# Performance work log

Hardware: AMD Instinct MI355X
Metric: run time of the kernel (lower is better)

The kernel has to match this reference:

```python
import jax, jax.numpy as jnp
import numpy as np

N, M, E, DIM, H = 50000, 50000, 640000, 128, 8
DH = DIM // H
EPS = 1e-5

def _prelu(x, alpha):
    return jnp.where(x >= 0, x, alpha * x)

def setup_inputs() -> dict:
    key0 = jax.random.key(0)
    ks = jax.random.split(key0, 12)
    s = 1.0 / np.sqrt(DIM)
    return {
        "query": jax.random.normal(ks[0], (N, DIM), jnp.float32),
        "key": jax.random.normal(ks[1], (M, DIM), jnp.float32),
        "value": jax.random.normal(ks[2], (M, DIM), jnp.float32),
        "query_idx": jax.random.randint(ks[3], (E,), 0, N),
        "key_idx": jax.random.randint(ks[4], (E,), 0, M),
        "Wq": jax.random.normal(ks[5], (DIM, DIM), jnp.float32) * s,
        "bq": jnp.zeros((DIM,), jnp.float32),
        "Wk": jax.random.normal(ks[6], (DIM, DIM), jnp.float32) * s,
        "bk": jnp.zeros((DIM,), jnp.float32),
        "Wv": jax.random.normal(ks[7], (DIM, DIM), jnp.float32) * s,
        "bv": jnp.zeros((DIM,), jnp.float32),
        "Wp": jax.random.normal(ks[8], (DIM, DIM), jnp.float32) * s,
        "bp": jnp.zeros((DIM,), jnp.float32),
        "a": jax.random.normal(ks[9], (1, H, DH), jnp.float32) * 0.1,
        "alpha": jnp.full((1,), 0.25, jnp.float32),
        "gamma": jnp.ones((DIM,), jnp.float32),
        "beta": jnp.zeros((DIM,), jnp.float32),
    }

def reference(query, key, value, query_idx, key_idx, Wq, bq, Wk, bk, Wv, bv, Wp, bp, a, alpha, gamma, beta):
    n = query.shape[0]
    # projections (node-level, then gather per edge; linear commutes with gather)
    Qq = query @ Wq + bq            # [N, DIM]
    Kq = query @ Wk + bk            # [N, DIM] (self-attn key)
    Kk = key @ Wk + bk              # [M, DIM]
    Vq = query @ Wv + bv            # [N, DIM]
    Vv = value @ Wv + bv            # [M, DIM]
    # self-attention score per query node: [N, H, 1]
    attn_qq = (a * _prelu(Qq + Kq, alpha).reshape(n, H, DH)).sum(-1, keepdims=True)
    # per-edge additive attention score: [E, H, 1]
    e_feat = _prelu(Qq[query_idx] + Kk[key_idx], alpha)
    attn_e = (a * e_feat.reshape(-1, H, DH)).sum(-1, keepdims=True)
    # stable softmax over irregular query groups (include self)
    max_attn = jax.lax.stop_gradient(attn_qq.at[query_idx].max(attn_e))
    exp_qq = jnp.exp(attn_qq - max_attn)                 # [N, H, 1]
    exp_e = jnp.exp(attn_e - max_attn[query_idx])        # [E, H, 1]
    denom = exp_qq.at[query_idx].add(exp_e)              # [N, H, 1]
    denom = jnp.where(denom == 0, 1.0, denom)
    # weighted value scatter-sum (value_idx == key_idx)
    msg = exp_qq * Vq.reshape(n, H, DH)
    msg = msg.at[query_idx].add(exp_e * Vv[key_idx].reshape(-1, H, DH))
    out = (msg / denom).reshape(n, DIM) @ Wp + bp
    res = query + out
    mu = res.mean(-1, keepdims=True)
    var = res.var(-1, keepdims=True)
    return gamma * (res - mu) / jnp.sqrt(var + EPS) + beta
```

## Files before the change

kernel.cpp:

```cpp
#include <hip/hip_runtime.h>
#include <math.h>

#define DIM 128
#define NH 8
#define LN_EPS 1e-5f
#define NEGINF -3.0e38f

using bf16x8 = __attribute__((ext_vector_type(8))) short;
using f32x4  = __attribute__((ext_vector_type(4))) float;

__device__ __forceinline__ float prelu_f(float x, float al) { return x >= 0.f ? x : al * x; }

__device__ __forceinline__ short f2bf(float f) {
    unsigned u = __float_as_uint(f);
    unsigned r = (u + 0x7fffu + ((u >> 16) & 1u)) >> 16;
    return (short)r;
}
__device__ __forceinline__ float bflo(unsigned u) { return __uint_as_float(u << 16); }
__device__ __forceinline__ float bfhi(unsigned u) { return __uint_as_float(u & 0xffff0000u); }

__device__ __forceinline__ unsigned cvt_pk_bf16(float lo, float hi) {
    unsigned r;
    asm("v_cvt_pk_bf16_f32 %0, %1, %2" : "=v"(r) : "v"(lo), "v"(hi));
    return r;
}

__device__ __forceinline__ float swz_xor1(float x) {
    return __int_as_float(__builtin_amdgcn_ds_swizzle(__float_as_int(x), 0x041F));
}
__device__ __forceinline__ float swz_xor2(float x) {
    return __int_as_float(__builtin_amdgcn_ds_swizzle(__float_as_int(x), 0x081F));
}
__device__ __forceinline__ float swz_xor16(float x) {
    return __int_as_float(__builtin_amdgcn_ds_swizzle(__float_as_int(x), 0x401F));
}
__device__ __forceinline__ float swz_xor32(float x) {
    return __shfl_xor(x, 32);
}

__global__ __launch_bounds__(256) void setup_kernel(
    const float* __restrict__ W0, const float* __restrict__ W1,
    const float* __restrict__ W2, const float* __restrict__ W3,
    short* __restrict__ P0, short* __restrict__ P1,
    short* __restrict__ P2, short* __restrict__ P3,
    const int* __restrict__ qidx, int* __restrict__ counts, int E)
{
    if (blockIdx.x < 32) {
        const int id = blockIdx.x * 256 + threadIdx.x;
        const int mat = id >> 11;
        const int rem = id & 2047;
        const int ks = rem >> 9;
        const int ct = (rem >> 6) & 7;
        const int lane = rem & 63;
        const int lr = lane & 15, lg = lane >> 4;
        const float* W = mat == 0 ? W0 : mat == 1 ? W1 : mat == 2 ? W2 : W3;
        short* P = mat == 0 ? P0 : mat == 1 ? P1 : mat == 2 ? P2 : P3;
        short v[8];
        #pragma unroll
        for (int r = 0; r < 8; ++r)
            v[r] = f2bf(W[(ks * 32 + lg * 8 + r) * DIM + ct * 16 + lr]);
        *(bf16x8*)&P[(size_t)((ks * 8 + ct) * 64 + lane) * 8] = *(bf16x8*)v;
    } else {
        const int b = blockIdx.x - 32;
        for (int e = b * 256 + threadIdx.x; e < E; e += 1024 * 256)
            atomicAdd(&counts[qidx[e]], 1);
    }
}

__global__ __launch_bounds__(256) void proj_all_mfma(
    const float* __restrict__ query,
    const float* __restrict__ key, const float* __restrict__ value,
    const short* __restrict__ Wqp, const short* __restrict__ Wkp, const short* __restrict__ Wvp,
    const float* __restrict__ bq, const float* __restrict__ bk, const float* __restrict__ bv,
    const float* __restrict__ avec, const float* __restrict__ alpha_p,
    short* __restrict__ QV16, float* __restrict__ attnqq4,
    short* __restrict__ KV16, int N, int M, int nb)
{
    __shared__ unsigned lds[4][16][66];
    const int wid = threadIdx.x >> 6, lane = threadIdx.x & 63;
    const int lr = lane & 15, lg = lane >> 4;
    const bool evenlane = (lane & 1) == 0;

    if ((int)blockIdx.x < nb) {
        const int row0 = ((int)blockIdx.x * 4 + wid) * 16;
        if (row0 >= N) return;
        const int arow = row0 + lr;
        const bool rowok = arow < N;

        bf16x8 afrag[4];
        #pragma unroll
        for (int ks = 0; ks < 4; ++ks) {
            float t[8] = {0.f,0.f,0.f,0.f,0.f,0.f,0.f,0.f};
            if (rowok) {
                *(float4*)&t[0] = *(const float4*)&query[(size_t)arow * DIM + ks * 32 + lg * 8];
                *(float4*)&t[4] = *(const float4*)&query[(size_t)arow * DIM + ks * 32 + lg * 8 + 4];
            }
            union { bf16x8 v; unsigned u[4]; } a;
            a.u[0] = cvt_pk_bf16(t[0], t[1]);
            a.u[1] = cvt_pk_bf16(t[2], t[3]);
            a.u[2] = cvt_pk_bf16(t[4], t[5]);
            a.u[3] = cvt_pk_bf16(t[6], t[7]);
            afrag[ks] = a.v;
        }
        const float al = alpha_p[0];
        unsigned* qvout = (unsigned*)QV16;

        #pragma unroll 2
        for (int ct = 0; ct < 8; ++ct) {
            f32x4 aq = (f32x4)0.f, ak = (f32x4)0.f;
            #pragma unroll
            for (int ks = 0; ks < 4; ++ks) {
                const size_t bo = (size_t)((ks * 8 + ct) * 64 + lane) * 8;
                aq = __builtin_amdgcn_mfma_f32_16x16x32_bf16(afrag[ks], *(const bf16x8*)&Wqp[bo], aq, 0, 0, 0);
                ak = __builtin_amdgcn_mfma_f32_16x16x32_bf16(afrag[ks], *(const bf16x8*)&Wkp[bo], ak, 0, 0, 0);
            }
            const int col = ct * 16 + lr;
            const float bqv = bq[col], bkv = bk[col], av = avec[col];
            #pragma unroll
            for (int r = 0; r < 4; ++r) {
                const int row = lg * 4 + r;
                const float qv = aq[r] + bqv;
                const float kv = ak[r] + bkv;
                float part = av * prelu_f(qv + kv, al);
                part += swz_xor1(part);
                part += swz_xor2(part);
                const int grow = row0 + row;
                if ((lr & 3) == 0 && grow < N)
                    attnqq4[(size_t)grow * 32 + ct * 4 + (lr >> 2)] = part;
                const float qn = swz_xor1(qv);
                if (evenlane) lds[wid][row][ct * 8 + (lr >> 1)] = cvt_pk_bf16(qv, qn);
            }
        }
        #pragma unroll
        for (int rr = 0; rr < 16; ++rr) {
            const int grow = row0 + rr;
            if (grow < N) qvout[(size_t)grow * 128 + lane] = lds[wid][rr][lane];
        }

        #pragma unroll 2
        for (int ct = 0; ct < 8; ++ct) {
            f32x4 acv = (f32x4)0.f;
            #pragma unroll
            for (int ks = 0; ks < 4; ++ks) {
                const size_t bo = (size_t)((ks * 8 + ct) * 64 + lane) * 8;
                acv = __builtin_amdgcn_mfma_f32_16x16x32_bf16(afrag[ks], *(const bf16x8*)&Wvp[bo], acv, 0, 0, 0);
            }
            const int col = ct * 16 + lr;
            const float bvv = bv[col];
            #pragma unroll
            for (int r = 0; r < 4; ++r) {
                const int row = lg * 4 + r;
                const float vv = acv[r] + bvv;
                const float vn = swz_xor1(vv);
                if (evenlane) lds[wid][row][ct * 8 + (lr >> 1)] = cvt_pk_bf16(vv, vn);
            }
        }
        #pragma unroll
        for (int rr = 0; rr < 16; ++rr) {
            const int grow = row0 + rr;
            if (grow < N) qvout[(size_t)grow * 128 + 64 + lane] = lds[wid][rr][lane];
        }
    } else {
        const int row0 = (((int)blockIdx.x - nb) * 4 + wid) * 16;
        if (row0 >= M) return;
        const int arow = row0 + lr;
        const bool rowok = arow < M;
        unsigned* kvout = (unsigned*)KV16;

        {
            bf16x8 afK[4];
            #pragma unroll
            for (int ks = 0; ks < 4; ++ks) {
                float t[8] = {0.f,0.f,0.f,0.f,0.f,0.f,0.f,0.f};
                if (rowok) {
                    *(float4*)&t[0] = *(const float4*)&key[(size_t)arow * DIM + ks * 32 + lg * 8];
                    *(float4*)&t[4] = *(const float4*)&key[(size_t)arow * DIM + ks * 32 + lg * 8 + 4];
                }
                union { bf16x8 v; unsigned u[4]; } a;
                a.u[0] = cvt_pk_bf16(t[0], t[1]);
                a.u[1] = cvt_pk_bf16(t[2], t[3]);
                a.u[2] = cvt_pk_bf16(t[4], t[5]);
                a.u[3] = cvt_pk_bf16(t[6], t[7]);
                afK[ks] = a.v;
            }
            #pragma unroll 2
            for (int ct = 0; ct < 8; ++ct) {
                f32x4 ack = (f32x4)0.f;
                #pragma unroll
                for (int ks = 0; ks < 4; ++ks) {
                    const size_t bo = (size_t)((ks * 8 + ct) * 64 + lane) * 8;
                    ack = __builtin_amdgcn_mfma_f32_16x16x32_bf16(afK[ks], *(const bf16x8*)&Wkp[bo], ack, 0, 0, 0);
                }
                const int col = ct * 16 + lr;
                const float bkv = bk[col];
                #pragma unroll
                for (int r = 0; r < 4; ++r) {
                    const int row = lg * 4 + r;
                    const float kv = ack[r] + bkv;
                    const float kn = swz_xor1(kv);
                    if (evenlane) lds[wid][row][ct * 8 + (lr >> 1)] = cvt_pk_bf16(kv, kn);
                }
            }
            #pragma unroll
            for (int rr = 0; rr < 16; ++rr) {
                const int grow = row0 + rr;
                if (grow < M) kvout[(size_t)grow * 128 + lane] = lds[wid][rr][lane];
            }
        }
        {
            bf16x8 afV[4];
            #pragma unroll
            for (int ks = 0; ks < 4; ++ks) {
                float t[8] = {0.f,0.f,0.f,0.f,0.f,0.f,0.f,0.f};
                if (rowok) {
                    *(float4*)&t[0] = *(const float4*)&value[(size_t)arow * DIM + ks * 32 + lg * 8];
                    *(float4*)&t[4] = *(const float4*)&value[(size_t)arow * DIM + ks * 32 + lg * 8 + 4];
                }
                union { bf16x8 v; unsigned u[4]; } a;
                a.u[0] = cvt_pk_bf16(t[0], t[1]);
                a.u[1] = cvt_pk_bf16(t[2], t[3]);
                a.u[2] = cvt_pk_bf16(t[4], t[5]);
                a.u[3] = cvt_pk_bf16(t[6], t[7]);
                afV[ks] = a.v;
            }
            #pragma unroll 2
            for (int ct = 0; ct < 8; ++ct) {
                f32x4 acv = (f32x4)0.f;
                #pragma unroll
                for (int ks = 0; ks < 4; ++ks) {
                    const size_t bo = (size_t)((ks * 8 + ct) * 64 + lane) * 8;
                    acv = __builtin_amdgcn_mfma_f32_16x16x32_bf16(afV[ks], *(const bf16x8*)&Wvp[bo], acv, 0, 0, 0);
                }
                const int col = ct * 16 + lr;
                const float bvv = bv[col];
                #pragma unroll
                for (int r = 0; r < 4; ++r) {
                    const int row = lg * 4 + r;
                    const float vv = acv[r] + bvv;
                    const float vn = swz_xor1(vv);
                    if (evenlane) lds[wid][row][ct * 8 + (lr >> 1)] = cvt_pk_bf16(vv, vn);
                }
            }
            #pragma unroll
            for (int rr = 0; rr < 16; ++rr) {
                const int grow = row0 + rr;
                if (grow < M) kvout[(size_t)grow * 128 + 64 + lane] = lds[wid][rr][lane];
            }
        }
    }
}

__global__ __launch_bounds__(256) void scan1_kernel(const int* __restrict__ counts,
                                                    int* __restrict__ bsum, int N)
{
    __shared__ int sh[256];
    int i = blockIdx.x * 256 + threadIdx.x;
    sh[threadIdx.x] = (i < N) ? counts[i] : 0;
    __syncthreads();
    #pragma unroll
    for (int off = 128; off; off >>= 1) {
        if (threadIdx.x < off) sh[threadIdx.x] += sh[threadIdx.x + off];
        __syncthreads();
    }
    if (threadIdx.x == 0) bsum[blockIdx.x] = sh[0];
}

__global__ __launch_bounds__(256) void scan2_kernel(const int* __restrict__ bsum,
                                                    int* __restrict__ boff, int B)
{
    int t = threadIdx.x;
    if (B > 256) {
        if (t == 0) { int run = 0; for (int i = 0; i < B; ++i) { int v = bsum[i]; boff[i] = run; run += v; } }
        return;
    }
    __shared__ int sh[256];
    int v = (t < B) ? bsum[t] : 0;
    sh[t] = v;
    __syncthreads();
    for (int off = 1; off < 256; off <<= 1) {
        int x = (t >= off) ? sh[t - off] : 0;
        __syncthreads();
        sh[t] += x;
        __syncthreads();
    }
    if (t < B) boff[t] = sh[t] - v;
}

__global__ __launch_bounds__(256) void scan3_kernel(const int* __restrict__ counts,
                                                    const int* __restrict__ boff,
                                                    int* __restrict__ offsets,
                                                    int* __restrict__ cursor,
                                                    int N, int E)
{
    __shared__ int sh[256];
    int t = threadIdx.x;
    int i = blockIdx.x * 256 + t;
    int v = (i < N) ? counts[i] : 0;
    sh[t] = v;
    __syncthreads();
    for (int off = 1; off < 256; off <<= 1) {
        int x = (t >= off) ? sh[t - off] : 0;
        __syncthreads();
        sh[t] += x;
        __syncthreads();
    }
    int base = boff[blockIdx.x];
    if (i < N) {
        int o = base + sh[t] - v;
        offsets[i] = o;
        cursor[i] = o;
    }
    if (i == 0) offsets[N] = E;
}

__global__ void fill_kernel(const int* __restrict__ qidx, const int* __restrict__ kidx,
                            int* __restrict__ cursor, int* __restrict__ ksorted, int E)
{
    for (int e = blockIdx.x * blockDim.x + threadIdx.x; e < E; e += gridDim.x * blockDim.x) {
        int q = qidx[e];
        int pos = atomicAdd(&cursor[q], 1);
        ksorted[pos] = kidx[e];
    }
}

__global__ __launch_bounds__(256) void edge_agg_kernel(
    const short* __restrict__ QV16, const float* __restrict__ attnqq4,
    const short* __restrict__ KV16,
    const int* __restrict__ ksorted, const int* __restrict__ offsets,
    const float* __restrict__ avec, const float* __restrict__ alpha_p,
    short* __restrict__ msgn16, int N)
{
    const int lane = threadIdx.x & 63;
    const int wid  = threadIdx.x >> 6;
    const int e    = lane >> 4;
    const int sub  = lane & 15;
    const int h    = sub >> 1;

    const float al = alpha_p[0];
    const float r  = (1.f - al) / (1.f + al);
    const float s1 = (1.f + al) * 0.5f;

    float c[8];
    {
        const float4 a0 = *(const float4*)&avec[sub * 8];
        const float4 a1 = *(const float4*)&avec[sub * 8 + 4];
        c[0] = a0.x * s1; c[1] = a0.y * s1; c[2] = a0.z * s1; c[3] = a0.w * s1;
        c[4] = a1.x * s1; c[5] = a1.y * s1; c[6] = a1.z * s1; c[7] = a1.w * s1;
    }

    const int wavesTotal = gridDim.x * 4;

    for (int n = blockIdx.x * 4 + wid; n < N; n += wavesTotal) {
        float q[8];
        {
            unsigned qd[4];
            *(uint4*)qd = *(const uint4*)&QV16[(size_t)n * 256 + sub * 8];
            #pragma unroll
            for (int j = 0; j < 4; ++j) { q[2*j] = bflo(qd[j]); q[2*j+1] = bfhi(qd[j]); }
        }

        float acc[8];
        float den;
        if (e == 0) {
            unsigned vdi[4];
            *(uint4*)vdi = *(const uint4*)&QV16[(size_t)n * 256 + 128 + sub * 8];
            #pragma unroll
            for (int j = 0; j < 4; ++j) { acc[2*j] = bflo(vdi[j]); acc[2*j+1] = bfhi(vdi[j]); }
            den = 1.f;
        } else {
            #pragma unroll
            for (int d = 0; d < 8; ++d) acc[d] = 0.f;
            den = 0.f;
        }

        float m;
        {
            const float4 a4 = *(const float4*)&attnqq4[(size_t)n * 32 + h * 4];
            m = (a4.x + a4.y) + (a4.z + a4.w);
        }

        const int p0 = offsets[n];
        const int p1 = offsets[n + 1];
        const int T  = (p1 - p0 + 3) >> 2;
        bool div = false;

        #define ROWLOAD(kd_, vd_, ki_)                                        \
            {                                                                 \
                const size_t kb = (size_t)(ki_) * 256 + sub * 8;              \
                *(uint4*)(kd_) = *(const uint4*)&KV16[kb];                    \
                *(uint4*)(vd_) = *(const uint4*)&KV16[kb + 128];              \
            }

        unsigned kdA[4], vdA[4], kdB[4], vdB[4];
        unsigned kdC[4], vdC[4], kdD[4], vdD[4];
        bool vA, vB, vC, vD;
        int kiA, kiB, kiC, kiD;

        {
            int i0 = p0 + e,      i1 = p0 + 4 + e;
            int i2 = p0 + 8 + e,  i3 = p0 + 12 + e;
            vA = i0 < p1; vB = i1 < p1; vC = i2 < p1; vD = i3 < p1;
            const int k0 = vA ? ksorted[i0] : 0;
            const int k1 = vB ? ksorted[i1] : 0;
            const int k2 = vC ? ksorted[i2] : 0;
            const int k3 = vD ? ksorted[i3] : 0;
            ROWLOAD(kdA, vdA, k0); ROWLOAD(kdB, vdB, k1);
            ROWLOAD(kdC, vdC, k2); ROWLOAD(kdD, vdD, k3);
            int j0 = p0 + 16 + e, j1 = p0 + 20 + e;
            int j2 = p0 + 24 + e, j3 = p0 + 28 + e;
            kiA = (j0 < p1) ? ksorted[j0] : 0;
            kiB = (j1 < p1) ? ksorted[j1] : 0;
            kiC = (j2 < p1) ? ksorted[j2] : 0;
            kiD = (j3 < p1) ? ksorted[j3] : 0;
        }

        #define COMPUTE(kd_, vd_, vflag)                                      \
            {                                                                 \
                float sp = 0.f;                                               \
                _Pragma("unroll")                                             \
                for (int j = 0; j < 4; ++j) {                                 \
                    const float x0 = q[2*j]   + bflo(kd_[j]);                 \
                    const float x1 = q[2*j+1] + bfhi(kd_[j]);                 \
                    const float t0 = fmaf(r, __builtin_fabsf(x0), x0);        \
                    const float t1 = fmaf(r, __builtin_fabsf(x1), x1);        \
                    sp = fmaf(c[2*j], t0, sp);                                \
                    sp = fmaf(c[2*j+1], t1, sp);                              \
                }                                                             \
                const float sf = sp + swz_xor1(sp);                           \
                const float s = (vflag) ? sf : NEGINF;                        \
                const float d_ = s - m;                                       \
                if (__any(d_ > 8.f)) {                                        \
                    div = true;                                               \
                    const float nm = fmaxf(m, s);                             \
                    const float cc = __expf(m - nm);                          \
                    const float w = __expf(s - nm);                           \
                    den = den * cc + w;                                       \
                    _Pragma("unroll")                                         \
                    for (int j = 0; j < 4; ++j) {                             \
                        acc[2*j]   = fmaf(acc[2*j],   cc, w * bflo(vd_[j])); \
                        acc[2*j+1] = fmaf(acc[2*j+1], cc, w * bfhi(vd_[j])); \
                    }                                                         \
                    m = nm;                                                   \
                } else {                                                      \
                    const float w = __expf(d_);                               \
                    den += w;                                                 \
                    _Pragma("unroll")                                         \
                    for (int j = 0; j < 4; ++j) {                             \
                        acc[2*j]   = fmaf(w, bflo(vd_[j]), acc[2*j]);         \
                        acc[2*j+1] = fmaf(w, bfhi(vd_[j]), acc[2*j+1]);       \
                    }                                                         \
                }                                                             \
            }

        #define RELOAD(kd_, vd_, vflag, ki_, st4, st8)                        \
            {                                                                 \
                vflag = (p0 + (st4) * 4 + e) < p1;                            \
                ROWLOAD(kd_, vd_, ki_);                                       \
                const int fi = p0 + (st8) * 4 + e;                            \
                ki_ = (fi < p1) ? ksorted[fi] : 0;                            \
            }

        #pragma unroll 1
        for (int t = 0; t < T; t += 4) {
            COMPUTE(kdA, vdA, vA); RELOAD(kdA, vdA, vA, kiA, t + 4, t + 8);
            COMPUTE(kdB, vdB, vB); RELOAD(kdB, vdB, vB, kiB, t + 5, t + 9);
            COMPUTE(kdC, vdC, vC); RELOAD(kdC, vdC, vC, kiC, t + 6, t + 10);
            COMPUTE(kdD, vdD, vD); RELOAD(kdD, vdD, vD, kiD, t + 7, t + 11);
        }
        #undef COMPUTE
        #undef RELOAD
        #undef ROWLOAD

        #define MERGE_ROUND(SWZ)                                    \
            {                                                       \
                const float m2 = SWZ(m);                            \
                const float den2 = SWZ(den);                        \
                const float nm = fmaxf(m, m2);                      \
                const float ca = __expf(m - nm);                    \
                const float cb = __expf(m2 - nm);                   \
                den = den * ca + den2 * cb;                         \
                _Pragma("unroll")                                   \
                for (int d = 0; d < 8; ++d)                         \
                    acc[d] = acc[d] * ca + SWZ(acc[d]) * cb;        \
                m = nm;                                             \
            }
        #define SUM_ROUND(SWZ)                                      \
            {                                                       \
                den += SWZ(den);                                    \
                _Pragma("unroll")                                   \
                for (int d = 0; d < 8; ++d) acc[d] += SWZ(acc[d]);  \
            }
        if (div) {
            MERGE_ROUND(swz_xor16);
            MERGE_ROUND(swz_xor32);
        } else {
            SUM_ROUND(swz_xor16);
            SUM_ROUND(swz_xor32);
        }
        #undef MERGE_ROUND
        #undef SUM_ROUND

        if (e == 0) {
            const float inv = 1.f / den;
            unsigned u[4];
            #pragma unroll
            for (int j = 0; j < 4; ++j)
                u[j] = cvt_pk_bf16(acc[2*j] * inv, acc[2*j+1] * inv);
            *(uint4*)&msgn16[(size_t)n * DIM + sub * 8] = *(uint4*)u;
        }
    }
}

__global__ __launch_bounds__(256) void out_ln_mfma(
    const short* __restrict__ msgn16, const short* __restrict__ Wpp,
    const float* __restrict__ bp, const float* __restrict__ query,
    const float* __restrict__ gamma, const float* __restrict__ beta,
    float* __restrict__ out, int N)
{
    __shared__ float ys[64][130];
    const int wid = threadIdx.x >> 6, lane = threadIdx.x & 63;
    const int rowbase = blockIdx.x * 64;
    const int row0 = rowbase + wid * 16;
    const int lr = lane & 15, lg = lane >> 4;

    if (row0 < N) {
        bf16x8 afrag[4];
        const int arow = row0 + lr;
        const bool rowok = arow < N;
        #pragma unroll
        for (int ks = 0; ks < 4; ++ks) {
            if (rowok)
                afrag[ks] = *(const bf16x8*)&msgn16[(size_t)arow * DIM + ks * 32 + lg * 8];
            else {
                bf16x8 z;
                #pragma unroll
                for (int j = 0; j < 8; ++j) z[j] = 0;
                afrag[ks] = z;
            }
        }
        #pragma unroll 2
        for (int ct = 0; ct < 8; ++ct) {
            f32x4 acc = (f32x4)0.f;
            #pragma unroll
            for (int ks = 0; ks < 4; ++ks) {
                const size_t bo = (size_t)((ks * 8 + ct) * 64 + lane) * 8;
                acc = __builtin_amdgcn_mfma_f32_16x16x32_bf16(afrag[ks], *(const bf16x8*)&Wpp[bo], acc, 0, 0, 0);
            }
            const int col = ct * 16 + lr;
            const float bpv = bp[col];
            #pragma unroll
            for (int r = 0; r < 4; ++r)
                ys[wid * 16 + lg * 4 + r][col] = acc[r] + bpv;
        }
    }
    __syncthreads();

    for (int rr = 0; rr < 16; ++rr) {
        const int r = wid * 16 + rr;
        const int grow = rowbase + r;
        if (grow >= N) break;
        const float y1 = ys[r][lane], y2 = ys[r][lane + 64];
        const float q1 = query[(size_t)grow * DIM + lane];
        const float q2 = query[(size_t)grow * DIM + lane + 64];
        const float r1 = y1 + q1, r2 = y2 + q2;
        float s = r1 + r2;
        float ss = r1 * r1 + r2 * r2;
        #pragma unroll
        for (int off = 32; off; off >>= 1) {
            s += __shfl_xor(s, off);
            ss += __shfl_xor(ss, off);
        }
        const float mu = s * (1.f / DIM);
        const float var = ss * (1.f / DIM) - mu * mu;
        const float rstd = rsqrtf(var + LN_EPS);
        out[(size_t)grow * DIM + lane] = gamma[lane] * (r1 - mu) * rstd + beta[lane];
        out[(size_t)grow * DIM + lane + 64] = gamma[lane + 64] * (r2 - mu) * rstd + beta[lane + 64];
    }
}

extern "C" void kernel_launch(void* const* d_in, const int* in_sizes, int n_in,
                              void* d_out, int out_size, void* d_ws, size_t ws_size,
                              hipStream_t stream) {
    const float* query = (const float*)d_in[0];
    const float* key   = (const float*)d_in[1];
    const float* value = (const float*)d_in[2];
    const int* query_idx = (const int*)d_in[3];
    const int* key_idx   = (const int*)d_in[4];
    const float* Wq = (const float*)d_in[5];
    const float* bq = (const float*)d_in[6];
    const float* Wk = (const float*)d_in[7];
    const float* bk = (const float*)d_in[8];
    const float* Wv = (const float*)d_in[9];
    const float* bv = (const float*)d_in[10];
    const float* Wp = (const float*)d_in[11];
    const float* bp = (const float*)d_in[12];
    const float* avec  = (const float*)d_in[13];
    const float* alpha = (const float*)d_in[14];
    const float* gamma = (const float*)d_in[15];
    const float* beta  = (const float*)d_in[16];
    float* out = (float*)d_out;

    const int N = in_sizes[0] / DIM;
    const int M = in_sizes[1] / DIM;
    const int E = in_sizes[3];

    float* f = (float*)d_ws;
    float* attnqq4 = f; f += (size_t)N * 32;
    short* sp = (short*)f;
    short* QV16 = sp;   sp += (size_t)N * 256;
    short* KV16 = sp;   sp += (size_t)M * 256;
    short* msgn16 = sp; sp += (size_t)N * DIM;
    short* Wqp = sp;    sp += DIM * DIM;
    short* Wkp = sp;    sp += DIM * DIM;
    short* Wvp = sp;    sp += DIM * DIM;
    short* Wpp = sp;    sp += DIM * DIM;
    int* ip = (int*)(((size_t)sp + 15) & ~(size_t)15);
    int* counts  = ip;  ip += N;
    int* offsets = ip;  ip += N + 1;
    int* cursor  = ip;  ip += N;
    int* bsum    = ip;  ip += 4096;
    int* boff    = ip;  ip += 4096;
    int* ksorted = ip;  ip += E;

    const int B = (N + 255) / 256;
    const int nb = (N + 63) / 64;
    const int mb = (M + 63) / 64;

    hipMemsetAsync(counts, 0, (size_t)N * sizeof(int), stream);

    setup_kernel<<<1056, 256, 0, stream>>>(Wq, Wk, Wv, Wp, Wqp, Wkp, Wvp, Wpp,
                                           query_idx, counts, E);

    scan1_kernel<<<B, 256, 0, stream>>>(counts, bsum, N);
    scan2_kernel<<<1, 256, 0, stream>>>(bsum, boff, B);
    scan3_kernel<<<B, 256, 0, stream>>>(counts, boff, offsets, cursor, N, E);
    fill_kernel<<<1024, 256, 0, stream>>>(query_idx, key_idx, cursor, ksorted, E);

    proj_all_mfma<<<nb + mb, 256, 0, stream>>>(
        query, key, value, Wqp, Wkp, Wvp, bq, bk, bv, avec, alpha,
        QV16, attnqq4, KV16, N, M, nb);

    edge_agg_kernel<<<2048, 256, 0, stream>>>(
        QV16, attnqq4, KV16, ksorted, offsets, avec, alpha, msgn16, N);

    out_ln_mfma<<<(N + 63) / 64, 256, 0, stream>>>(
        msgn16, Wpp, bp, query, gamma, beta, out, N);
}
```

Before: 205.6 us.

## Move self-attention score into edge kernel, store Q/Kq/V as packed bf16 rows

The projection kernel no longer computes the per-node self-attention score. Instead it writes Qq, Kq and Vq as one bf16 row of 384 elements, and the edge aggregation kernel recomputes the score from Qq+Kq using the abs-based PReLU form. The key/value branch is also merged, so K and V are computed together in one pass through an LDS tile with a single store loop, and edge row loads use 32-bit byte offsets. This drops the fp32 attnqq4 buffer and the swizzle reductions in the projection kernel, in exchange for an extra 256 bytes read per node in the edge kernel and narrow 16-bit LDS stores.

```diff
diff --git a/kernel.cpp b/kernel.cpp
--- a/kernel.cpp
+++ b/kernel.cpp
@@ -9,8 +9,6 @@
 using bf16x8 = __attribute__((ext_vector_type(8))) short;
 using f32x4  = __attribute__((ext_vector_type(4))) float;
 
-__device__ __forceinline__ float prelu_f(float x, float al) { return x >= 0.f ? x : al * x; }
-
 __device__ __forceinline__ short f2bf(float f) {
     unsigned u = __float_as_uint(f);
     unsigned r = (u + 0x7fffu + ((u >> 16) & 1u)) >> 16;
@@ -27,9 +25,6 @@
 
 __device__ __forceinline__ float swz_xor1(float x) {
     return __int_as_float(__builtin_amdgcn_ds_swizzle(__float_as_int(x), 0x041F));
-}
-__device__ __forceinline__ float swz_xor2(float x) {
-    return __int_as_float(__builtin_amdgcn_ds_swizzle(__float_as_int(x), 0x081F));
 }
 __device__ __forceinline__ float swz_xor16(float x) {
     return __int_as_float(__builtin_amdgcn_ds_swizzle(__float_as_int(x), 0x401F));
@@ -72,14 +67,11 @@
     const float* __restrict__ key, const float* __restrict__ value,
     const short* __restrict__ Wqp, const short* __restrict__ Wkp, const short* __restrict__ Wvp,
     const float* __restrict__ bq, const float* __restrict__ bk, const float* __restrict__ bv,
-    const float* __restrict__ avec, const float* __restrict__ alpha_p,
-    short* __restrict__ QV16, float* __restrict__ attnqq4,
-    short* __restrict__ KV16, int N, int M, int nb)
-{
-    __shared__ unsigned lds[4][16][66];
+    short* __restrict__ QKV16, short* __restrict__ KV16, int N, int M, int nb)
+{
+    __shared__ short tile[4][16][260];
     const int wid = threadIdx.x >> 6, lane = threadIdx.x & 63;
     const int lr = lane & 15, lg = lane >> 4;
-    const bool evenlane = (lane & 1) == 0;
 
     if ((int)blockIdx.x < nb) {
         const int row0 = ((int)blockIdx.x * 4 + wid) * 16;
@@ -102,8 +94,7 @@
             a.u[3] = cvt_pk_bf16(t[6], t[7]);
             afrag[ks] = a.v;
         }
-        const float al = alpha_p[0];
-        unsigned* qvout = (unsigned*)QV16;
+        unsigned* qkvout = (unsigned*)QKV16;
 
         #pragma unroll 2
         for (int ct = 0; ct < 8; ++ct) {
@@ -115,26 +106,25 @@
                 ak = __builtin_amdgcn_mfma_f32_16x16x32_bf16(afrag[ks], *(const bf16x8*)&Wkp[bo], ak, 0, 0, 0);
             }
             const int col = ct * 16 + lr;
-            const float bqv = bq[col], bkv = bk[col], av = avec[col];
+            const float bqv = bq[col], bkv = bk[col];
             #pragma unroll
             for (int r = 0; r < 4; ++r) {
                 const int row = lg * 4 + r;
-                const float qv = aq[r] + bqv;
-                const float kv = ak[r] + bkv;
-                float part = av * prelu_f(qv + kv, al);
-                part += swz_xor1(part);
-                part += swz_xor2(part);
-                const int grow = row0 + row;
-                if ((lr & 3) == 0 && grow < N)
-                    attnqq4[(size_t)grow * 32 + ct * 4 + (lr >> 2)] = part;
-                const float qn = swz_xor1(qv);
-                if (evenlane) lds[wid][row][ct * 8 + (lr >> 1)] = cvt_pk_bf16(qv, qn);
+                tile[wid][row][col]       = (short)cvt_pk_bf16(aq[r] + bqv, 0.f);
+                tile[wid][row][128 + col] = (short)cvt_pk_bf16(ak[r] + bkv, 0.f);
             }
         }
         #pragma unroll
         for (int rr = 0; rr < 16; ++rr) {
             const int grow = row0 + rr;
-            if (grow < N) qvout[(size_t)grow * 128 + lane] = lds[wid][rr][lane];
+            if (grow < N) {
+                #pragma unroll
+                for (int s = 0; s < 2; ++s) {
+                    const short2 pr = *(const short2*)&tile[wid][rr][s * 128 + lane * 2];
+                    qkvout[(size_t)grow * 192 + s * 64 + lane] =
+                        (unsigned)(unsigned short)pr.x | ((unsigned)(unsigned short)pr.y << 16);
+                }
+            }
         }
 
         #pragma unroll 2
@@ -148,17 +138,17 @@
             const int col = ct * 16 + lr;
             const float bvv = bv[col];
             #pragma unroll
-            for (int r = 0; r < 4; ++r) {
-                const int row = lg * 4 + r;
-                const float vv = acv[r] + bvv;
-                const float vn = swz_xor1(vv);
-                if (evenlane) lds[wid][row][ct * 8 + (lr >> 1)] = cvt_pk_bf16(vv, vn);
-            }
+            for (int r = 0; r < 4; ++r)
+                tile[wid][lg * 4 + r][col] = (short)cvt_pk_bf16(acv[r] + bvv, 0.f);
         }
         #pragma unroll
         for (int rr = 0; rr < 16; ++rr) {
             const int grow = row0 + rr;
-            if (grow < N) qvout[(size_t)grow * 128 + 64 + lane] = lds[wid][rr][lane];
+            if (grow < N) {
+                const short2 pr = *(const short2*)&tile[wid][rr][lane * 2];
+                qkvout[(size_t)grow * 192 + 128 + lane] =
+                    (unsigned)(unsigned short)pr.x | ((unsigned)(unsigned short)pr.y << 16);
+            }
         }
     } else {
         const int row0 = (((int)blockIdx.x - nb) * 4 + wid) * 16;
@@ -167,84 +157,57 @@
         const bool rowok = arow < M;
         unsigned* kvout = (unsigned*)KV16;
 
-        {
-            bf16x8 afK[4];
+        bf16x8 afK[4], afV[4];
+        #pragma unroll
+        for (int ks = 0; ks < 4; ++ks) {
+            float tk[8] = {0.f,0.f,0.f,0.f,0.f,0.f,0.f,0.f};
+            float tv[8] = {0.f,0.f,0.f,0.f,0.f,0.f,0.f,0.f};
+            if (rowok) {
+                *(float4*)&tk[0] = *(const float4*)&key[(size_t)arow * DIM + ks * 32 + lg * 8];
+                *(float4*)&tk[4] = *(const float4*)&key[(size_t)arow * DIM + ks * 32 + lg * 8 + 4];
+                *(float4*)&tv[0] = *(const float4*)&value[(size_t)arow * DIM + ks * 32 + lg * 8];
+                *(float4*)&tv[4] = *(const float4*)&value[(size_t)arow * DIM + ks * 32 + lg * 8 + 4];
+            }
+            union { bf16x8 v; unsigned u[4]; } a, b;
+            a.u[0] = cvt_pk_bf16(tk[0], tk[1]);
+            a.u[1] = cvt_pk_bf16(tk[2], tk[3]);
+            a.u[2] = cvt_pk_bf16(tk[4], tk[5]);
+            a.u[3] = cvt_pk_bf16(tk[6], tk[7]);
+            b.u[0] = cvt_pk_bf16(tv[0], tv[1]);
+            b.u[1] = cvt_pk_bf16(tv[2], tv[3]);
+            b.u[2] = cvt_pk_bf16(tv[4], tv[5]);
+            b.u[3] = cvt_pk_bf16(tv[6], tv[7]);
+            afK[ks] = a.v; afV[ks] = b.v;
+        }
+
+        #pragma unroll 2
+        for (int ct = 0; ct < 8; ++ct) {
+            f32x4 ack = (f32x4)0.f, acv = (f32x4)0.f;
             #pragma unroll
             for (int ks = 0; ks < 4; ++ks) {
-                float t[8] = {0.f,0.f,0.f,0.f,0.f,0.f,0.f,0.f};
-                if (rowok) {
-                    *(float4*)&t[0] = *(const float4*)&key[(size_t)arow * DIM + ks * 32 + lg * 8];
-                    *(float4*)&t[4] = *(const float4*)&key[(size_t)arow * DIM + ks * 32 + lg * 8 + 4];
+                const size_t bo = (size_t)((ks * 8 + ct) * 64 + lane) * 8;
+                ack = __builtin_amdgcn_mfma_f32_16x16x32_bf16(afK[ks], *(const bf16x8*)&Wkp[bo], ack, 0, 0, 0);
+                acv = __builtin_amdgcn_mfma_f32_16x16x32_bf16(afV[ks], *(const bf16x8*)&Wvp[bo], acv, 0, 0, 0);
+            }
+            const int col = ct * 16 + lr;
+            const float bkv = bk[col], bvv = bv[col];
+            #pragma unroll
+            for (int r = 0; r < 4; ++r) {
+                const int row = lg * 4 + r;
+                tile[wid][row][col]       = (short)cvt_pk_bf16(ack[r] + bkv, 0.f);
+                tile[wid][row][128 + col] = (short)cvt_pk_bf16(acv[r] + bvv, 0.f);
+            }
+        }
+        #pragma unroll
+        for (int rr = 0; rr < 16; ++rr) {
+            const int grow = row0 + rr;
+            if (grow < M) {
+                #pragma unroll
+                for (int s = 0; s < 2; ++s) {
+                    const short2 pr = *(const short2*)&tile[wid][rr][s * 128 + lane * 2];
+                    kvout[(size_t)grow * 128 + s * 64 + lane] =
+                        (unsigned)(unsigned short)pr.x | ((unsigned)(unsigned short)pr.y << 16);
                 }
-                union { bf16x8 v; unsigned u[4]; } a;
-                a.u[0] = cvt_pk_bf16(t[0], t[1]);
-                a.u[1] = cvt_pk_bf16(t[2], t[3]);
-                a.u[2] = cvt_pk_bf16(t[4], t[5]);
-                a.u[3] = cvt_pk_bf16(t[6], t[7]);
-                afK[ks] = a.v;
-            }
-            #pragma unroll 2
-            for (int ct = 0; ct < 8; ++ct) {
-                f32x4 ack = (f32x4)0.f;
-                #pragma unroll
-                for (int ks = 0; ks < 4; ++ks) {
-                    const size_t bo = (size_t)((ks * 8 + ct) * 64 + lane) * 8;
-                    ack = __builtin_amdgcn_mfma_f32_16x16x32_bf16(afK[ks], *(const bf16x8*)&Wkp[bo], ack, 0, 0, 0);
-                }
-                const int col = ct * 16 + lr;
-                const float bkv = bk[col];
-                #pragma unroll
-                for (int r = 0; r < 4; ++r) {
-                    const int row = lg * 4 + r;
-                    const float kv = ack[r] + bkv;
-                    const float kn = swz_xor1(kv);
-                    if (evenlane) lds[wid][row][ct * 8 + (lr >> 1)] = cvt_pk_bf16(kv, kn);
-                }
-            }
-            #pragma unroll
-            for (int rr = 0; rr < 16; ++rr) {
-                const int grow = row0 + rr;
-                if (grow < M) kvout[(size_t)grow * 128 + lane] = lds[wid][rr][lane];
-            }
-        }
-        {
-            bf16x8 afV[4];
-            #pragma unroll
-            for (int ks = 0; ks < 4; ++ks) {
-                float t[8] = {0.f,0.f,0.f,0.f,0.f,0.f,0.f,0.f};
-                if (rowok) {
-                    *(float4*)&t[0] = *(const float4*)&value[(size_t)arow * DIM + ks * 32 + lg * 8];
-                    *(float4*)&t[4] = *(const float4*)&value[(size_t)arow * DIM + ks * 32 + lg * 8 + 4];
-                }
-                union { bf16x8 v; unsigned u[4]; } a;
-                a.u[0] = cvt_pk_bf16(t[0], t[1]);
-                a.u[1] = cvt_pk_bf16(t[2], t[3]);
-                a.u[2] = cvt_pk_bf16(t[4], t[5]);
-                a.u[3] = cvt_pk_bf16(t[6], t[7]);
-                afV[ks] = a.v;
-            }
-            #pragma unroll 2
-            for (int ct = 0; ct < 8; ++ct) {
-                f32x4 acv = (f32x4)0.f;
-                #pragma unroll
-                for (int ks = 0; ks < 4; ++ks) {
-                    const size_t bo = (size_t)((ks * 8 + ct) * 64 + lane) * 8;
-                    acv = __builtin_amdgcn_mfma_f32_16x16x32_bf16(afV[ks], *(const bf16x8*)&Wvp[bo], acv, 0, 0, 0);
-                }
-                const int col = ct * 16 + lr;
-                const float bvv = bv[col];
-                #pragma unroll
-                for (int r = 0; r < 4; ++r) {
-                    const int row = lg * 4 + r;
-                    const float vv = acv[r] + bvv;
-                    const float vn = swz_xor1(vv);
-                    if (evenlane) lds[wid][row][ct * 8 + (lr >> 1)] = cvt_pk_bf16(vv, vn);
-                }
-            }
-            #pragma unroll
-            for (int rr = 0; rr < 16; ++rr) {
-                const int grow = row0 + rr;
-                if (grow < M) kvout[(size_t)grow * 128 + 64 + lane] = lds[wid][rr][lane];
             }
         }
     }
@@ -324,7 +287,7 @@
 }
 
 __global__ __launch_bounds__(256) void edge_agg_kernel(
-    const short* __restrict__ QV16, const float* __restrict__ attnqq4,
+    const short* __restrict__ QKV16,
     const short* __restrict__ KV16,
     const int* __restrict__ ksorted, const int* __restrict__ offsets,
     const float* __restrict__ avec, const float* __restrict__ alpha_p,
@@ -334,7 +297,6 @@
     const int wid  = threadIdx.x >> 6;
     const int e    = lane >> 4;
     const int sub  = lane & 15;
-    const int h    = sub >> 1;
 
     const float al = alpha_p[0];
     const float r  = (1.f - al) / (1.f + al);
@@ -348,22 +310,39 @@
         c[4] = a1.x * s1; c[5] = a1.y * s1; c[6] = a1.z * s1; c[7] = a1.w * s1;
     }
 
+    const char* KVb = (const char*)KV16;
+    const unsigned subB = (unsigned)(sub * 16);
     const int wavesTotal = gridDim.x * 4;
 
     for (int n = blockIdx.x * 4 + wid; n < N; n += wavesTotal) {
         float q[8];
         {
             unsigned qd[4];
-            *(uint4*)qd = *(const uint4*)&QV16[(size_t)n * 256 + sub * 8];
+            *(uint4*)qd = *(const uint4*)&QKV16[(size_t)n * 384 + sub * 8];
             #pragma unroll
             for (int j = 0; j < 4; ++j) { q[2*j] = bflo(qd[j]); q[2*j+1] = bfhi(qd[j]); }
+        }
+
+        float m;
+        {
+            unsigned kq[4];
+            *(uint4*)kq = *(const uint4*)&QKV16[(size_t)n * 384 + 128 + sub * 8];
+            float sp = 0.f;
+            #pragma unroll
+            for (int j = 0; j < 4; ++j) {
+                const float x0 = q[2*j]   + bflo(kq[j]);
+                const float x1 = q[2*j+1] + bfhi(kq[j]);
+                sp = fmaf(c[2*j],   fmaf(r, __builtin_fabsf(x0), x0), sp);
+                sp = fmaf(c[2*j+1], fmaf(r, __builtin_fabsf(x1), x1), sp);
+            }
+            m = sp + swz_xor1(sp);
         }
 
         float acc[8];
         float den;
         if (e == 0) {
             unsigned vdi[4];
-            *(uint4*)vdi = *(const uint4*)&QV16[(size_t)n * 256 + 128 + sub * 8];
+            *(uint4*)vdi = *(const uint4*)&QKV16[(size_t)n * 384 + 256 + sub * 8];
             #pragma unroll
             for (int j = 0; j < 4; ++j) { acc[2*j] = bflo(vdi[j]); acc[2*j+1] = bfhi(vdi[j]); }
             den = 1.f;
@@ -371,12 +350,6 @@
             #pragma unroll
             for (int d = 0; d < 8; ++d) acc[d] = 0.f;
             den = 0.f;
-        }
-
-        float m;
-        {
-            const float4 a4 = *(const float4*)&attnqq4[(size_t)n * 32 + h * 4];
-            m = (a4.x + a4.y) + (a4.z + a4.w);
         }
 
         const int p0 = offsets[n];
@@ -386,9 +359,9 @@
 
         #define ROWLOAD(kd_, vd_, ki_)                                        \
             {                                                                 \
-                const size_t kb = (size_t)(ki_) * 256 + sub * 8;              \
-                *(uint4*)(kd_) = *(const uint4*)&KV16[kb];                    \
-                *(uint4*)(vd_) = *(const uint4*)&KV16[kb + 128];              \
+                const unsigned ob = (unsigned)(ki_) * 512u + subB;            \
+                *(uint4*)(kd_) = *(const uint4*)(KVb + ob);                   \
+                *(uint4*)(vd_) = *(const uint4*)(KVb + ob + 256);             \
             }
 
         unsigned kdA[4], vdA[4], kdB[4], vdB[4];
@@ -604,10 +577,8 @@
     const int M = in_sizes[1] / DIM;
     const int E = in_sizes[3];
 
-    float* f = (float*)d_ws;
-    float* attnqq4 = f; f += (size_t)N * 32;
-    short* sp = (short*)f;
-    short* QV16 = sp;   sp += (size_t)N * 256;
+    short* sp = (short*)d_ws;
+    short* QKV16 = sp;  sp += (size_t)N * 384;
     short* KV16 = sp;   sp += (size_t)M * 256;
     short* msgn16 = sp; sp += (size_t)N * DIM;
     short* Wqp = sp;    sp += DIM * DIM;
@@ -637,11 +608,11 @@
     fill_kernel<<<1024, 256, 0, stream>>>(query_idx, key_idx, cursor, ksorted, E);
 
     proj_all_mfma<<<nb + mb, 256, 0, stream>>>(
-        query, key, value, Wqp, Wkp, Wvp, bq, bk, bv, avec, alpha,
-        QV16, attnqq4, KV16, N, M, nb);
+        query, key, value, Wqp, Wkp, Wvp, bq, bk, bv,
+        QKV16, KV16, N, M, nb);
 
     edge_agg_kernel<<<2048, 256, 0, stream>>>(
-        QV16, attnqq4, KV16, ksorted, offsets, avec, alpha, msgn16, N);
+        QKV16, KV16, ksorted, offsets, avec, alpha, msgn16, N);
 
     out_ln_mfma<<<(N + 63) / 64, 256, 0, stream>>>(
         msgn16, Wpp, bp, query, gamma, beta, out, N);
```

After: 209.5 us. Within noise of the previous version (+1.9%).
